# Performance work log

Measured on AMD Instinct MI355X. Metric: run time of the kernel, lower is better.

The kernel has to match this reference:

```python
import jax, jax.numpy as jnp
import numpy as np

FS, R, ULAW = 160, 2, 256  # frame_size, n_samples_per_step, 2**ulaw


def _conv1d(x, w, b):
    # x: [B,C,L], w: [O,I,3], VALID conv (PyTorch Conv1d, no padding)
    y = jax.lax.conv_general_dilated(x, w, (1,), 'VALID',
                                     dimension_numbers=('NCH', 'OIH', 'NCH'))
    return y + b[None, :, None]


def _gru(x, Wih, Whh, bih, bhh):
    # PyTorch GRU (batch_first), gate order r,z,n. x: [B,T,In] -> [B,T,H]
    B = x.shape[0]
    H = Whh.shape[1]
    xW = jnp.einsum('bti,gi->btg', x, Wih) + bih  # precompute input gates [B,T,3H]
    def step(h, xw):
        gh = h @ Whh.T + bhh
        r = jax.nn.sigmoid(xw[:, :H] + gh[:, :H])
        z = jax.nn.sigmoid(xw[:, H:2 * H] + gh[:, H:2 * H])
        n = jnp.tanh(xw[:, 2 * H:] + r * gh[:, 2 * H:])
        h = (1.0 - z) * n + z * h
        return h, h
    h0 = jnp.zeros((B, H), x.dtype)
    _, ys = jax.lax.scan(step, h0, jnp.swapaxes(xW, 0, 1))
    return jnp.swapaxes(ys, 0, 1)


def _mdense(x, w1, w2, b1, b2, f1, f2):
    return jnp.tanh(x @ w1.T + b1) * f1 + jnp.tanh(x @ w2.T + b2) * f2


def setup_inputs() -> dict:
    key = jax.random.key(0)
    ks = jax.random.split(key, 40)
    B, NF, NBF = 64, 15, 20
    T = (NF - 4) * FS  # 1760: two VALID k=3 convs -> 11 frames
    EP, ES, DF, H1, H2 = 64, 128, 128, 384, 16
    IN_A = 3 * ES * R + DF   # 896
    IN_B = H1 + DF           # 512
    p = lambda k, shape, s=0.1: (s * jax.random.normal(k, shape)).astype(jnp.float32)
    d = {
        'in_data': jax.random.randint(ks[0], (B, T, 3), 0, ULAW),
        'features': jax.random.normal(ks[1], (B, NF, NBF), jnp.float32),
        'periods': jax.random.randint(ks[2], (B, NF, 1), 0, 256),
        'targets': jax.random.randint(ks[3], (B, T), 0, ULAW),
        'embed_pitch': p(ks[4], (256, EP)),
        'embed_sig': p(ks[5], (ULAW, ES)),
        'conv1_w': p(ks[6], (DF, EP + NBF, 3)), 'conv1_b': p(ks[7], (DF,)),
        'conv2_w': p(ks[8], (DF, DF, 3)), 'conv2_b': p(ks[9], (DF,)),
        'fd1_w': p(ks[10], (DF, DF)), 'fd1_b': p(ks[11], (DF,)),
        'fd2_w': p(ks[12], (DF, DF)), 'fd2_b': p(ks[13], (DF,)),
        'ga_wih': p(ks[14], (3 * H1, IN_A)), 'ga_whh': p(ks[15], (3 * H1, H1)),
        'ga_bih': p(ks[16], (3 * H1,)), 'ga_bhh': p(ks[17], (3 * H1,)),
        'gb_wih': p(ks[18], (3 * H2, IN_B)), 'gb_whh': p(ks[19], (3 * H2, H2)),
        'gb_bih': p(ks[20], (3 * H2,)), 'gb_bhh': p(ks[21], (3 * H2,)),
        'md1_w1': p(ks[22], (ULAW, H2)), 'md1_w2': p(ks[23], (ULAW, H2)),
        'md1_b1': p(ks[24], (ULAW,)), 'md1_b2': p(ks[25], (ULAW,)),
        'md1_f1': jnp.ones((ULAW,), jnp.float32), 'md1_f2': jnp.ones((ULAW,), jnp.float32),
        'md2_w1': p(ks[26], (ULAW, H2 + ES)), 'md2_w2': p(ks[27], (ULAW, H2 + ES)),
        'md2_b1': p(ks[28], (ULAW,)), 'md2_b2': p(ks[29], (ULAW,)),
        'md2_f1': jnp.ones((ULAW,), jnp.float32), 'md2_f2': jnp.ones((ULAW,), jnp.float32),
    }
    return d


def reference(in_data, features, periods, targets, embed_pitch, embed_sig,
              conv1_w, conv1_b, conv2_w, conv2_b, fd1_w, fd1_b, fd2_w, fd2_b,
              ga_wih, ga_whh, ga_bih, ga_bhh, gb_wih, gb_whh, gb_bih, gb_bhh,
              md1_w1, md1_w2, md1_b1, md1_b2, md1_f1, md1_f2,
              md2_w1, md2_w2, md2_b1, md2_b2, md2_f1, md2_f2):
    B, T = targets.shape
    # frame-rate feature network
    pitch = embed_pitch[periods[..., 0]]                  # [B,15,EP]
    cat = jnp.concatenate([features, pitch], axis=-1)      # [B,15,NBF+EP]
    x = jnp.swapaxes(cat, 1, 2)                            # [B,C,15]
    x = jnp.tanh(_conv1d(x, conv1_w, conv1_b))
    x = jnp.tanh(_conv1d(x, conv2_w, conv2_b))             # [B,DF,11]
    f = jnp.swapaxes(x, 1, 2)
    f = jnp.tanh(f @ fd1_w.T + fd1_b)
    f = jnp.tanh(f @ fd2_w.T + fd2_b)                      # [B,11,DF]
    rep = jnp.repeat(f, FS // R, axis=1)                   # [B,880,DF]
    # sample-rate network (bunched: R samples per step)
    emb = embed_sig[in_data].reshape(B, T, -1).reshape(B, T // R, -1)  # [B,880,3*ES*R]
    rnn_in = jnp.concatenate([emb, rep], axis=-1)
    g1 = _gru(rnn_in, ga_wih, ga_whh, ga_bih, ga_bhh)      # [B,880,H1]
    g2 = _gru(jnp.concatenate([g1, rep], axis=-1), gb_wih, gb_whh, gb_bih, gb_bhh)  # [B,880,H2]
    o1 = _mdense(g2, md1_w1, md1_w2, md1_b1, md1_b2, md1_f1, md1_f2)  # [B,880,ULAW]
    # teacher forcing (p_teacher_forcing = 1.0): even-index targets feed branch 2
    pred_exc = targets[:, 0::R]                            # [B,880]
    ctx = jnp.concatenate([g2, embed_sig[pred_exc]], axis=-1)
    o2 = _mdense(ctx, md2_w1, md2_w2, md2_b1, md2_b2, md2_f1, md2_f2)
    # strided scatter: out[:, ::2]=o1, out[:, 1::2]=o2 == interleave
    out = jnp.stack([o1, o2], axis=2).reshape(B, T, ULAW)
    return out
```

## Files before the change

kernel.cpp:

```cpp
#include <hip/hip_runtime.h>
#include <hip/hip_bf16.h>
#include <hip/hip_fp16.h>

#define NF    15
#define NBF   20
#define TT    1760
#define TS    880
#define EP    64
#define ES    128
#define DF    128
#define H1    384
#define G3    1152
#define INA   896
#define JREP  11

typedef _Float16 h2v __attribute__((ext_vector_type(2)));
typedef unsigned long long u64;

__device__ __forceinline__ float sigmf_(float x){ return 1.0f/(1.0f + __expf(-x)); }
__device__ __forceinline__ float tanhf_(float x){ return 2.0f/(1.0f + __expf(-2.0f*x)) - 1.0f; }
__device__ __forceinline__ h2v bc_h2(unsigned u){ return __builtin_bit_cast(h2v, u); }
__device__ __forceinline__ float fdot2_(h2v a, h2v b, float c){
#if __has_builtin(__builtin_amdgcn_fdot2)
  return __builtin_amdgcn_fdot2(a, b, c, false);
#else
  return c + (float)a[0]*(float)b[0] + (float)a[1]*(float)b[1];
#endif
}
__device__ __forceinline__ unsigned pk2_(float a, float b){
#if __has_builtin(__builtin_amdgcn_cvt_pkrtz)
  return __builtin_bit_cast(unsigned, __builtin_amdgcn_cvt_pkrtz(a, b));
#else
  unsigned lo = (unsigned)__builtin_bit_cast(unsigned short, (_Float16)a);
  unsigned hi = (unsigned)__builtin_bit_cast(unsigned short, (_Float16)b);
  return lo | (hi << 16);
#endif
}
__device__ __forceinline__ void bar_lgkm(){
  asm volatile("s_waitcnt lgkmcnt(0)" ::: "memory");
  __builtin_amdgcn_s_barrier();
  __builtin_amdgcn_sched_barrier(0);
}

__global__ __launch_bounds__(128) void k_frame(const float* feat, const int* periods, const float* embp,
   const float* c1w, const float* c1b, const float* c2w, const float* c2b,
   const float* f1w, const float* f1b, const float* f2w, const float* f2b, float* fout)
{
  __shared__ float cat[NF*84];
  __shared__ float x1[13*DF];
  __shared__ float x2[JREP*DF];
  int b = blockIdx.x, tid = threadIdx.x;
  for (int idx = tid; idx < NF*84; idx += 128){
    int j = idx/84, c = idx%84;
    cat[idx] = (c < NBF) ? feat[(b*NF+j)*NBF + c]
                         : embp[periods[b*NF+j]*EP + (c-NBF)];
  }
  __syncthreads();
  int o = tid;
  for (int p = 0; p < 13; ++p){
    float acc = c1b[o];
    for (int kk = 0; kk < 3; ++kk)
      for (int c = 0; c < 84; ++c)
        acc += cat[(p+kk)*84 + c] * c1w[(o*84+c)*3+kk];
    x1[p*DF+o] = tanhf_(acc);
  }
  __syncthreads();
  for (int p = 0; p < JREP; ++p){
    float acc = c2b[o];
    for (int kk = 0; kk < 3; ++kk)
      for (int c = 0; c < DF; ++c)
        acc += x1[(p+kk)*DF+c] * c2w[(o*DF+c)*3+kk];
    x2[p*DF+o] = tanhf_(acc);
  }
  __syncthreads();
  for (int p = 0; p < JREP; ++p){
    float acc = f1b[o];
    for (int c = 0; c < DF; ++c) acc += x2[p*DF+c]*f1w[o*DF+c];
    x1[p*DF+o] = tanhf_(acc);
  }
  __syncthreads();
  for (int p = 0; p < JREP; ++p){
    float acc = f2b[o];
    for (int c = 0; c < DF; ++c) acc += x1[p*DF+c]*f2w[o*DF+c];
    fout[(b*JREP+p)*DF+o] = tanhf_(acc);
  }
}

__global__ __launch_bounds__(256) void k_wpack5(const float* whh, _Float16* wpk){
  int o = blockIdx.x*256 + threadIdx.x;
  int hu = o & 1;
  int c  = (o >> 1) & 3;
  int idx = o >> 3;
  int tid = idx % 768;
  int n   = (idx / 768) % 18;
  int hf  = idx / (768*18);
  int i = tid % 384, u = tid / 384;
  int gd = n*4 + c;
  int m = gd / 12, dc = gd % 12;
  int pos  = (dc % 2) + 2*(dc / 6);
  int gate = (dc % 6) >> 1;
  int j = hf*96 + u*48 + (4*m + pos)*2 + hu;
  wpk[o] = (_Float16)whh[(gate*H1 + i)*H1 + j];
}

__global__ __launch_bounds__(256) void k_tables(const float* wih, const float* emb, float* GA){
  __shared__ float Wl[64*129];
  int k = blockIdx.x/18, g0 = (blockIdx.x%18)*64;
  int tid = threadIdx.x;
  for (int idx = tid; idx < 64*128; idx += 256){
    int gg = idx>>7, c = idx&127;
    Wl[gg*129+c] = wih[(size_t)(g0+gg)*INA + k*128 + c];
  }
  __syncthreads();
  int vv = tid>>6, gg = tid&63;
  for (int v = vv; v < 256; v += 4){
    const float* e = emb + (size_t)v*ES;
    float acc = 0.f;
    for (int c = 0; c < 128; ++c) acc += e[c]*Wl[gg*129+c];
    GA[(size_t)(k*256+v)*G3 + g0+gg] = acc;
  }
}

__global__ __launch_bounds__(256) void k_xwrepA(const float* wih, const float* f,
                                                const float* bih, const float* bhh, float* xwA){
  __shared__ float Wl[64*129];
  int g0 = blockIdx.x*64, tid = threadIdx.x;
  for (int idx = tid; idx < 64*128; idx += 256){
    int gg = idx>>7, c = idx&127;
    Wl[gg*129+c] = wih[(size_t)(g0+gg)*INA + 768 + c];
  }
  __syncthreads();
  int vv = tid>>6, gg = tid&63; int g = g0+gg;
  float badd = bih[g] + (g < 768 ? bhh[g] : 0.f);
  for (int row = vv; row < 64*JREP; row += 4){
    const float* fr = f + (size_t)row*DF;
    float acc = badd;
    for (int c = 0; c < 128; ++c) acc += fr[c]*Wl[gg*129+c];
    xwA[(size_t)row*G3 + g] = acc;
  }
}

__global__ __launch_bounds__(256) void k_xwrepB(const float* wih, const float* f,
                                                const float* bih, const float* bhh, float* xwB){
  __shared__ float Wl[48*129];
  int b = blockIdx.x, tid = threadIdx.x;
  for (int idx = tid; idx < 48*128; idx += 256){
    int r = idx>>7, c = idx&127;
    Wl[r*129+c] = wih[r*512 + 384 + c];
  }
  __syncthreads();
  for (int idx = tid; idx < JREP*48; idx += 256){
    int j = idx/48, r = idx%48;
    const float* fr = f + (size_t)(b*JREP+j)*DF;
    float acc = bih[r] + (r < 32 ? bhh[r] : 0.f);
    for (int c = 0; c < 128; ++c) acc += fr[c]*Wl[r*129+c];
    xwB[(size_t)(b*JREP+j)*48 + r] = acc;
  }
}

__global__ __launch_bounds__(256) void k_t2(const float* w1, const float* w2, const float* emb, float* T2){
  __shared__ float Wl[64*129];
  int tbl = blockIdx.x>>2; int c0 = (blockIdx.x&3)*64; int tid = threadIdx.x;
  const float* w = tbl ? w2 : w1;
  for (int idx = tid; idx < 64*128; idx += 256){
    int cc = idx>>7, e = idx&127;
    Wl[cc*129+e] = w[(c0+cc)*144 + 16 + e];
  }
  __syncthreads();
  int vv = tid>>6, cc = tid&63;
  for (int v = vv; v < 256; v += 4){
    const float* e = emb + (size_t)v*ES;
    float acc = 0.f;
    for (int c = 0; c < 128; ++c) acc += e[c]*Wl[cc*129+c];
    T2[tbl*65536 + v*256 + c0+cc] = acc;
  }
}

#define LD18(n) uint4 d##n = wsrc[(size_t)(n)*768];
#define Q2(A,B,C, q2) { \
  h2v hA = hh[jb2 + (q2)*2],     hB = hh[jb2 + (q2)*2 + 1]; \
  ar = fdot2_(hA, bc_h2(A.x), ar); ar = fdot2_(hB, bc_h2(A.y), ar); \
  az = fdot2_(hA, bc_h2(A.z), az); az = fdot2_(hB, bc_h2(A.w), az); \
  an = fdot2_(hA, bc_h2(B.x), an); an = fdot2_(hB, bc_h2(B.y), an); \
  h2v hC = hh[jb2 + (q2)*2 + 2], hD = hh[jb2 + (q2)*2 + 3]; \
  ar = fdot2_(hC, bc_h2(B.z), ar); ar = fdot2_(hD, bc_h2(B.w), ar); \
  az = fdot2_(hC, bc_h2(C.x), az); az = fdot2_(hD, bc_h2(C.y), az); \
  an = fdot2_(hC, bc_h2(C.z), an); an = fdot2_(hD, bc_h2(C.w), an); }
#define DOTS12 \
  Q2(d0,d1,d2,0) Q2(d3,d4,d5,2) Q2(d6,d7,d8,4) \
  Q2(d9,d10,d11,6) Q2(d12,d13,d14,8) Q2(d15,d16,d17,10)

#define PL2(na, nb_, p) { u64 w2 = __hip_atomic_load((const u64*)(p), __ATOMIC_RELAXED, __HIP_MEMORY_SCOPE_AGENT); \
  rv##na = (unsigned)w2; rv##nb_ = (unsigned)(w2 >> 32); \
  ok &= ((rv##na & 1023u) == tg) & ((rv##nb_ & 1023u) == tg); }

__global__ __launch_bounds__(768, 3) void k_scanA13(const int* __restrict__ in_data,
        const float* __restrict__ GA, const float* __restrict__ xwA,
        const uint4* __restrict__ wpk, const float* __restrict__ bhh,
        unsigned* __restrict__ g1u, unsigned* pbuf)
{
  __shared__ __align__(16) unsigned h16u[48];
  __shared__ __align__(8)  float pg[3][2][384];
  __shared__ __align__(8)  float xwb[2][G3];
  __shared__ int indr[2][8];
  const int P = blockIdx.x;
  const int b = P & 63, hf = P >> 6;
  const int tid = threadIdx.x;
  const int i  = tid % 384;
  const int u  = tid / 384;
  const int jb2 = u * 24;
  const int* ind_b = in_data + (size_t)b*TT*3;

  const uint4* wsrc = wpk + (size_t)(hf*18)*768 + tid;
  LD18(0) LD18(1) LD18(2) LD18(3) LD18(4) LD18(5) LD18(6) LD18(7) LD18(8)
  LD18(9) LD18(10) LD18(11) LD18(12) LD18(13) LD18(14) LD18(15) LD18(16) LD18(17)

  const bool isGat = (tid < 576);
  const int  c0 = 2*tid, c1 = 2*tid + 1;
  const bool isPub = (tid >= 96 && tid < 672);
  const int  po0 = 2*(tid - 96);

  float hreg0 = 0.f, hreg1 = 0.f, bn0 = 0.f, bn1 = 0.f;
  if (tid < 48){
    bn0 = bhh[768 + hf*96 + 2*tid];
    bn1 = bhh[768 + hf*96 + 2*tid + 1];
    h16u[tid] = 0u;
  }
  if (isGat){
    float s0 = xwA[(size_t)(b*JREP)*G3 + c0];
    float s1 = xwA[(size_t)(b*JREP)*G3 + c1];
    #pragma unroll
    for (int k2 = 0; k2 < 6; ++k2){
      int v = ind_b[k2];
      s0 += GA[((size_t)k2*256 + v)*G3 + c0];
      s1 += GA[((size_t)k2*256 + v)*G3 + c1];
    }
    xwb[0][c0] = s0; xwb[0][c1] = s1;
  }
  if (tid >= 576 && tid < 582) indr[1][tid-576] = ind_b[6 + (tid-576)];

  unsigned* pbo = pbuf + ((size_t)(b*4 + hf)*2)*G3;
  const int pf1 = (hf+1)&3, pf2 = (hf+2)&3, pf3 = (hf+3)&3;
  const unsigned* pb1 = pbuf + ((size_t)(b*4 + pf1)*2)*G3 + hf*96 + 2*(tid<48?tid:0);
  const unsigned* pb2 = pbuf + ((size_t)(b*4 + pf2)*2)*G3 + hf*96 + 2*(tid<48?tid:0);
  const unsigned* pb3 = pbuf + ((size_t)(b*4 + pf3)*2)*G3 + hf*96 + 2*(tid<48?tid:0);
  const h2v* hh = (const h2v*)h16u;
  __syncthreads();

  for (int t = 0; t < TS; ++t){
    const int nb = t & 1;
    const int tp = t + 1;
    float ga0=0.f,ga1=0.f,ga2=0.f,ga3=0.f,ga4=0.f,ga5=0.f,gx0=0.f;
    float gb0=0.f,gb1=0.f,gb2=0.f,gb3=0.f,gb4=0.f,gb5=0.f,gx1=0.f;
    if (tp < TS && isGat){
      int v0=indr[tp&1][0], v1=indr[tp&1][1], v2=indr[tp&1][2];
      int v3=indr[tp&1][3], v4=indr[tp&1][4], v5=indr[tp&1][5];
      const float* xwr = xwA + ((size_t)(b*JREP) + tp/80)*G3;
      ga0 = GA[((size_t)0*256 + v0)*G3 + c0]; gb0 = GA[((size_t)0*256 + v0)*G3 + c1];
      ga1 = GA[((size_t)1*256 + v1)*G3 + c0]; gb1 = GA[((size_t)1*256 + v1)*G3 + c1];
      ga2 = GA[((size_t)2*256 + v2)*G3 + c0]; gb2 = GA[((size_t)2*256 + v2)*G3 + c1];
      ga3 = GA[((size_t)3*256 + v3)*G3 + c0]; gb3 = GA[((size_t)3*256 + v3)*G3 + c1];
      ga4 = GA[((size_t)4*256 + v4)*G3 + c0]; gb4 = GA[((size_t)4*256 + v4)*G3 + c1];
      ga5 = GA[((size_t)5*256 + v5)*G3 + c0]; gb5 = GA[((size_t)5*256 + v5)*G3 + c1];
      gx0 = xwr[c0]; gx1 = xwr[c1];
    }
    int iv = 0;
    const int stg = t + 2;
    const bool doStg = (tid >= 576 && tid < 582 && stg < TS);
    if (doStg) iv = ind_b[6*stg + (tid-576)];
    float ar=0.f, az=0.f, an=0.f;
    DOTS12
    pg[0][u][i] = ar; pg[1][u][i] = az; pg[2][u][i] = an;
    if (tp < TS && isGat){
      xwb[tp&1][c0] = ga0+ga1+ga2+ga3+ga4+ga5+gx0;
      xwb[tp&1][c1] = gb0+gb1+gb2+gb3+gb4+gb5+gx1;
    }
    if (doStg) indr[t&1][tid-576] = iv;
    bar_lgkm();
    if (isPub){
      int g = po0/384, ii = po0 - g*384;
      float2 p0 = *(const float2*)&pg[g][0][ii];
      float2 p1 = *(const float2*)&pg[g][1][ii];
      float v0 = p0.x + p1.x, v1 = p0.y + p1.y;
      unsigned tw0 = (__builtin_bit_cast(unsigned, v0) & 0xFFFFFC00u) | (unsigned)(t & 1023);
      unsigned tw1 = (__builtin_bit_cast(unsigned, v1) & 0xFFFFFC00u) | (unsigned)(t & 1023);
      unsigned* dst = pbo + (size_t)nb*G3 + po0;
      __hip_atomic_store(dst,     tw0, __ATOMIC_RELAXED, __HIP_MEMORY_SCOPE_AGENT);
      __hip_atomic_store(dst + 1, tw1, __ATOMIC_RELAXED, __HIP_MEMORY_SCOPE_AGENT);
    } else if (tid < 48){
      const unsigned tg = (unsigned)t & 1023u;
      const unsigned* q1 = pb1 + (size_t)nb*G3;
      const unsigned* q2 = pb2 + (size_t)nb*G3;
      const unsigned* q3 = pb3 + (size_t)nb*G3;
      unsigned rv0,rv1,rv2,rv3,rv4,rv5,rv6,rv7,rv8;
      unsigned rv9,rv10,rv11,rv12,rv13,rv14,rv15,rv16,rv17;
      bool ok;
      do {
        ok = true;
        PL2(0,1,   q1+0) PL2(2,3,   q1+384) PL2(4,5,   q1+768)
        PL2(6,7,   q2+0) PL2(8,9,   q2+384) PL2(10,11, q2+768)
        PL2(12,13, q3+0) PL2(14,15, q3+384) PL2(16,17, q3+768)
        if (!ok) __builtin_amdgcn_s_sleep(1);
      } while (!ok);
      __builtin_amdgcn_sched_barrier(0);
      #define FV(n) __builtin_bit_cast(float, rv##n & 0xFFFFFC00u)
      int i0 = hf*96 + 2*tid;
      float2 o0 = *(const float2*)&pg[0][0][i0];  float2 o0b = *(const float2*)&pg[0][1][i0];
      float2 o1 = *(const float2*)&pg[1][0][i0];  float2 o1b = *(const float2*)&pg[1][1][i0];
      float2 o2 = *(const float2*)&pg[2][0][i0];  float2 o2b = *(const float2*)&pg[2][1][i0];
      float2 xr = *(const float2*)&xwb[nb][i0];
      float2 xz = *(const float2*)&xwb[nb][384 + i0];
      float2 xn = *(const float2*)&xwb[nb][768 + i0];
      float R0 = o0.x + o0b.x + FV(0)  + FV(6)  + FV(12) + xr.x;
      float R1 = o0.y + o0b.y + FV(1)  + FV(7)  + FV(13) + xr.y;
      float Z0 = o1.x + o1b.x + FV(2)  + FV(8)  + FV(14) + xz.x;
      float Z1 = o1.y + o1b.y + FV(3)  + FV(9)  + FV(15) + xz.y;
      float G0 = o2.x + o2b.x + FV(4)  + FV(10) + FV(16) + bn0;
      float G1 = o2.y + o2b.y + FV(5)  + FV(11) + FV(17) + bn1;
      #undef FV
      float rr0 = sigmf_(R0), zz0 = sigmf_(Z0);
      float nn0 = tanhf_(xn.x + rr0*G0);
      float h0 = (1.f - zz0)*nn0 + zz0*hreg0; hreg0 = h0;
      float rr1 = sigmf_(R1), zz1 = sigmf_(Z1);
      float nn1 = tanhf_(xn.y + rr1*G1);
      float h1 = (1.f - zz1)*nn1 + zz1*hreg1; hreg1 = h1;
      unsigned pack = pk2_(h0, h1);
      h16u[tid] = pack;
      g1u[((size_t)b*TS + t)*192 + hf*48 + tid] = pack;
    }
    bar_lgkm();
  }
}

__global__ __launch_bounds__(256) void k_xwB(const unsigned* g1u, const float* wih,
                                             const float* xwrB, float* xwB){
  __shared__ __align__(16) unsigned gl[16*194];
  __shared__ __align__(16) unsigned wl[48*194];
  int bi = blockIdx.x; int b = bi/55; int t0 = (bi%55)*16; int tid = threadIdx.x;
  for (int idx = tid; idx < 48*192; idx += 256){
    int r = idx/192, cp = idx%192;
    wl[r*194+cp] = pk2_(wih[r*512 + 2*cp], wih[r*512 + 2*cp + 1]);
  }
  for (int idx = tid; idx < 16*192; idx += 256){
    int tt = idx/192, c = idx%192;
    gl[tt*194+c] = g1u[((size_t)b*TS + t0+tt)*192 + c];
  }
  __syncthreads();
  int rr = tid>>4, tt = tid&15;
  int t = t0+tt;
  const float* xr = xwrB + ((size_t)(b*JREP) + t/80)*48;
  const h2v* gp = (const h2v*)&gl[tt*194];
  for (int rb = 0; rb < 3; ++rb){
    int r = rb*16 + rr;
    const h2v* wp_ = (const h2v*)&wl[r*194];
    float acc = 0.f;
    #pragma unroll 8
    for (int c = 0; c < 192; ++c) acc = fdot2_(gp[c], wp_[c], acc);
    xwB[((size_t)b*TS + t)*48 + r] = acc + xr[r];
  }
}

__global__ __launch_bounds__(64) void k_scanB(const float* xwB, const float* whh,
                                              const float* bhh, float* g2){
  int b = blockIdx.x, tid = threadIdx.x;
  float w0=0,w1=0,w2=0,w3=0,w4=0,w5=0,w6=0,w7=0;
  float w8=0,w9=0,w10=0,w11=0,w12=0,w13=0,w14=0,w15=0;
  if (tid < 48){
    const float* wr = whh + tid*16;
    w0=wr[0];w1=wr[1];w2=wr[2];w3=wr[3];w4=wr[4];w5=wr[5];w6=wr[6];w7=wr[7];
    w8=wr[8];w9=wr[9];w10=wr[10];w11=wr[11];w12=wr[12];w13=wr[13];w14=wr[14];w15=wr[15];
  }
  float bng = (tid < 16) ? bhh[32 + tid] : 0.f;
  float hv = 0.f;
  float xw_n = (tid < 48) ? xwB[(size_t)b*TS*48 + tid] : 0.f;
  for (int t = 0; t < TS; ++t){
    float xw = xw_n;
    if (t+1 < TS && tid < 48) xw_n = xwB[((size_t)b*TS + t+1)*48 + tid];
    float gh = 0.f;
    gh += w0 *__shfl(hv, 0, 64);  gh += w1 *__shfl(hv, 1, 64);
    gh += w2 *__shfl(hv, 2, 64);  gh += w3 *__shfl(hv, 3, 64);
    gh += w4 *__shfl(hv, 4, 64);  gh += w5 *__shfl(hv, 5, 64);
    gh += w6 *__shfl(hv, 6, 64);  gh += w7 *__shfl(hv, 7, 64);
    gh += w8 *__shfl(hv, 8, 64);  gh += w9 *__shfl(hv, 9, 64);
    gh += w10*__shfl(hv,10, 64);  gh += w11*__shfl(hv,11, 64);
    gh += w12*__shfl(hv,12, 64);  gh += w13*__shfl(hv,13, 64);
    gh += w14*__shfl(hv,14, 64);  gh += w15*__shfl(hv,15, 64);
    float val = xw + gh;
    float zv  = __shfl(val, (tid+16) & 63, 64);
    float xn_ = __shfl(xw,  (tid+32) & 63, 64);
    float gn_ = __shfl(gh,  (tid+32) & 63, 64) + bng;
    if (tid < 16){
      float r = sigmf_(val), z = sigmf_(zv);
      float n = tanhf_(xn_ + r*gn_);
      hv = (1.f - z)*n + z*hv;
      g2[((size_t)b*TS + t)*16 + tid] = hv;
    }
  }
}

__global__ __launch_bounds__(256) void k_out(const float* g2, const int* targets, const float* T2,
    const float* m1w1, const float* m1w2, const float* m1b1, const float* m1b2,
    const float* m1f1, const float* m1f2,
    const float* m2w1, const float* m2w2, const float* m2b1, const float* m2b2,
    const float* m2f1, const float* m2f2, float* out)
{
  __shared__ float wA[256*17], wB[256*17], wC[256*17], wD[256*17];
  __shared__ float g2l[16*16];
  int bi = blockIdx.x; int b = bi/55; int t0 = (bi%55)*16; int c = threadIdx.x;
  for (int d = 0; d < 16; ++d){
    wA[c*17+d] = m1w1[c*16+d];  wB[c*17+d] = m1w2[c*16+d];
    wC[c*17+d] = m2w1[c*144+d]; wD[c*17+d] = m2w2[c*144+d];
  }
  { int tt = c>>4, d = c&15; g2l[c] = g2[((size_t)b*TS + t0+tt)*16 + d]; }
  __syncthreads();
  float b1a = m1b1[c], b2a = m1b2[c], f1a = m1f1[c], f2a = m1f2[c];
  float b1b = m2b1[c], b2b = m2b2[c], f1b = m2f1[c], f2b = m2f2[c];
  for (int tt = 0; tt < 16; ++tt){
    int t = t0+tt;
    float d1 = b1a, d2 = b2a, e1 = b1b, e2 = b2b;
    for (int d = 0; d < 16; ++d){
      float g = g2l[tt*16+d];
      d1 += g*wA[c*17+d]; d2 += g*wB[c*17+d];
      e1 += g*wC[c*17+d]; e2 += g*wD[c*17+d];
    }
    int v = targets[b*TT + 2*t];
    e1 += T2[v*256+c]; e2 += T2[65536 + v*256+c];
    float o1 = f1a*tanhf_(d1) + f2a*tanhf_(d2);
    float o2 = f1b*tanhf_(e1) + f2b*tanhf_(e2);
    size_t base = ((size_t)b*TS + t)*2*256;
    out[base + c]       = o1;
    out[base + 256 + c] = o2;
  }
}

extern "C" void kernel_launch(void* const* d_in, const int* in_sizes, int n_in,
                              void* d_out, int out_size, void* d_ws, size_t ws_size,
                              hipStream_t stream) {
  const int*   in_data = (const int*)  d_in[0];
  const float* feat    = (const float*)d_in[1];
  const int*   periods = (const int*)  d_in[2];
  const int*   targets = (const int*)  d_in[3];
  const float* embp    = (const float*)d_in[4];
  const float* embs    = (const float*)d_in[5];
  const float* c1w = (const float*)d_in[6];  const float* c1b = (const float*)d_in[7];
  const float* c2w = (const float*)d_in[8];  const float* c2b = (const float*)d_in[9];
  const float* f1w = (const float*)d_in[10]; const float* f1b = (const float*)d_in[11];
  const float* f2w = (const float*)d_in[12]; const float* f2b = (const float*)d_in[13];
  const float* ga_wih = (const float*)d_in[14]; const float* ga_whh = (const float*)d_in[15];
  const float* ga_bih = (const float*)d_in[16]; const float* ga_bhh = (const float*)d_in[17];
  const float* gb_wih = (const float*)d_in[18]; const float* gb_whh = (const float*)d_in[19];
  const float* gb_bih = (const float*)d_in[20]; const float* gb_bhh = (const float*)d_in[21];
  const float* m1w1 = (const float*)d_in[22]; const float* m1w2 = (const float*)d_in[23];
  const float* m1b1 = (const float*)d_in[24]; const float* m1b2 = (const float*)d_in[25];
  const float* m1f1 = (const float*)d_in[26]; const float* m1f2 = (const float*)d_in[27];
  const float* m2w1 = (const float*)d_in[28]; const float* m2w2 = (const float*)d_in[29];
  const float* m2b1 = (const float*)d_in[30]; const float* m2b2 = (const float*)d_in[31];
  const float* m2f1 = (const float*)d_in[32]; const float* m2f2 = (const float*)d_in[33];
  float* out = (float*)d_out;

  float* GA     = (float*)d_ws;
  float* xWrepA = GA     + 1769472;
  float* xWrepB = xWrepA + 811008;
  float* fbuf   = xWrepB + 33792;
  float* xWB    = fbuf   + 90112;
  float* g2buf  = xWB    + 2703360;
  float* T2     = g2buf  + 901120;
  _Float16* Wpk = (_Float16*)(T2 + 131072);
  unsigned* pbuf = (unsigned*)(Wpk + 442368);
  _Float16* g1  = (_Float16*)d_out;

  (void)hipMemsetAsync(pbuf, 0xFF, 589824*sizeof(unsigned), stream);
  hipLaunchKernelGGL(k_frame, dim3(64), dim3(128), 0, stream,
                     feat, periods, embp, c1w, c1b, c2w, c2b, f1w, f1b, f2w, f2b, fbuf);
  hipLaunchKernelGGL(k_wpack5, dim3(1728), dim3(256), 0, stream, ga_whh, Wpk);
  hipLaunchKernelGGL(k_tables, dim3(108), dim3(256), 0, stream, ga_wih, embs, GA);
  hipLaunchKernelGGL(k_t2, dim3(8), dim3(256), 0, stream, m2w1, m2w2, embs, T2);
  hipLaunchKernelGGL(k_xwrepA, dim3(18), dim3(256), 0, stream, ga_wih, fbuf, ga_bih, ga_bhh, xWrepA);
  hipLaunchKernelGGL(k_xwrepB, dim3(64), dim3(256), 0, stream, gb_wih, fbuf, gb_bih, gb_bhh, xWrepB);
  hipLaunchKernelGGL(k_scanA13, dim3(256), dim3(768), 0, stream,
                     in_data, GA, xWrepA, (const uint4*)Wpk, ga_bhh,
                     (unsigned*)g1, pbuf);
  hipLaunchKernelGGL(k_xwB, dim3(64*55), dim3(256), 0, stream,
                     (const unsigned*)g1, gb_wih, xWrepB, xWB);
  hipLaunchKernelGGL(k_scanB, dim3(64), dim3(64), 0, stream, xWB, gb_whh, gb_bhh, g2buf);
  hipLaunchKernelGGL(k_out, dim3(64*55), dim3(256), 0, stream,
                     g2buf, targets, T2, m1w1, m1w2, m1b1, m1b2, m1f1, m1f2,
                     m2w1, m2w2, m2b1, m2b2, m2f1, m2f2, out);
}
```

Before: 3.645 ms.

## Fuse GRU-B input projection into scan A and merge setup kernels

Each GRU-A block now computes partial projections of its slice of the hidden state onto the GRU-B input weights inside the recurrent loop, one step late, using idle threads 48-95. It writes per-quarter partial sums that scan B adds up. This removes the g1 round trip through memory and the separate k_xwB kernel. The six small setup kernels are also merged into two launches with block-index dispatch. The trade-offs are extra shared memory and work on the latency-critical scan-A loop, and four partial-sum reads per step in scan B.

```diff
diff --git a/kernel.cpp b/kernel.cpp
--- a/kernel.cpp
+++ b/kernel.cpp
@@ -42,137 +42,148 @@
   __builtin_amdgcn_sched_barrier(0);
 }
 
-__global__ __launch_bounds__(128) void k_frame(const float* feat, const int* periods, const float* embp,
+__global__ __launch_bounds__(256) void k_setupA(const float* feat, const int* periods, const float* embp,
    const float* c1w, const float* c1b, const float* c2w, const float* c2b,
-   const float* f1w, const float* f1b, const float* f2w, const float* f2b, float* fout)
+   const float* f1w, const float* f1b, const float* f2w, const float* f2b, float* fout,
+   const float* whh, _Float16* wpk,
+   const float* wih, const float* emb, float* GA,
+   const float* m2w1, const float* m2w2, float* T2)
 {
-  __shared__ float cat[NF*84];
-  __shared__ float x1[13*DF];
-  __shared__ float x2[JREP*DF];
-  int b = blockIdx.x, tid = threadIdx.x;
-  for (int idx = tid; idx < NF*84; idx += 128){
-    int j = idx/84, c = idx%84;
-    cat[idx] = (c < NBF) ? feat[(b*NF+j)*NBF + c]
-                         : embp[periods[b*NF+j]*EP + (c-NBF)];
-  }
-  __syncthreads();
-  int o = tid;
-  for (int p = 0; p < 13; ++p){
-    float acc = c1b[o];
-    for (int kk = 0; kk < 3; ++kk)
-      for (int c = 0; c < 84; ++c)
-        acc += cat[(p+kk)*84 + c] * c1w[(o*84+c)*3+kk];
-    x1[p*DF+o] = tanhf_(acc);
-  }
-  __syncthreads();
-  for (int p = 0; p < JREP; ++p){
-    float acc = c2b[o];
-    for (int kk = 0; kk < 3; ++kk)
-      for (int c = 0; c < DF; ++c)
-        acc += x1[(p+kk)*DF+c] * c2w[(o*DF+c)*3+kk];
-    x2[p*DF+o] = tanhf_(acc);
-  }
-  __syncthreads();
-  for (int p = 0; p < JREP; ++p){
-    float acc = f1b[o];
-    for (int c = 0; c < DF; ++c) acc += x2[p*DF+c]*f1w[o*DF+c];
-    x1[p*DF+o] = tanhf_(acc);
-  }
-  __syncthreads();
-  for (int p = 0; p < JREP; ++p){
-    float acc = f2b[o];
-    for (int c = 0; c < DF; ++c) acc += x1[p*DF+c]*f2w[o*DF+c];
-    fout[(b*JREP+p)*DF+o] = tanhf_(acc);
-  }
-}
-
-__global__ __launch_bounds__(256) void k_wpack5(const float* whh, _Float16* wpk){
-  int o = blockIdx.x*256 + threadIdx.x;
-  int hu = o & 1;
-  int c  = (o >> 1) & 3;
-  int idx = o >> 3;
-  int tid = idx % 768;
-  int n   = (idx / 768) % 18;
-  int hf  = idx / (768*18);
-  int i = tid % 384, u = tid / 384;
-  int gd = n*4 + c;
-  int m = gd / 12, dc = gd % 12;
-  int pos  = (dc % 2) + 2*(dc / 6);
-  int gate = (dc % 6) >> 1;
-  int j = hf*96 + u*48 + (4*m + pos)*2 + hu;
-  wpk[o] = (_Float16)whh[(gate*H1 + i)*H1 + j];
-}
-
-__global__ __launch_bounds__(256) void k_tables(const float* wih, const float* emb, float* GA){
+  __shared__ float sh[8256];
+  const int bi = blockIdx.x, tid = threadIdx.x;
+  if (bi < 64){
+    float* cat = sh;
+    float* x1  = sh + 1260;
+    float* x2  = sh + 2924;
+    int b = bi;
+    for (int idx = tid; idx < NF*84; idx += 256){
+      int j = idx/84, c = idx%84;
+      cat[idx] = (c < NBF) ? feat[(b*NF+j)*NBF + c]
+                           : embp[periods[b*NF+j]*EP + (c-NBF)];
+    }
+    __syncthreads();
+    int o = tid;
+    if (o < DF){
+      for (int p = 0; p < 13; ++p){
+        float acc = c1b[o];
+        for (int kk = 0; kk < 3; ++kk)
+          for (int c = 0; c < 84; ++c)
+            acc += cat[(p+kk)*84 + c] * c1w[(o*84+c)*3+kk];
+        x1[p*DF+o] = tanhf_(acc);
+      }
+    }
+    __syncthreads();
+    if (o < DF){
+      for (int p = 0; p < JREP; ++p){
+        float acc = c2b[o];
+        for (int kk = 0; kk < 3; ++kk)
+          for (int c = 0; c < DF; ++c)
+            acc += x1[(p+kk)*DF+c] * c2w[(o*DF+c)*3+kk];
+        x2[p*DF+o] = tanhf_(acc);
+      }
+    }
+    __syncthreads();
+    if (o < DF){
+      for (int p = 0; p < JREP; ++p){
+        float acc = f1b[o];
+        for (int c = 0; c < DF; ++c) acc += x2[p*DF+c]*f1w[o*DF+c];
+        x1[p*DF+o] = tanhf_(acc);
+      }
+    }
+    __syncthreads();
+    if (o < DF){
+      for (int p = 0; p < JREP; ++p){
+        float acc = f2b[o];
+        for (int c = 0; c < DF; ++c) acc += x1[p*DF+c]*f2w[o*DF+c];
+        fout[(b*JREP+p)*DF+o] = tanhf_(acc);
+      }
+    }
+  } else if (bi < 1792){
+    int o = (bi-64)*256 + tid;
+    int hu = o & 1;
+    int c  = (o >> 1) & 3;
+    int idx = o >> 3;
+    int t768 = idx % 768;
+    int n    = (idx / 768) % 18;
+    int hf   = idx / (768*18);
+    int i = t768 % 384, u = t768 / 384;
+    int gd = n*4 + c;
+    int m = gd / 12, dc = gd % 12;
+    int pos  = (dc % 2) + 2*(dc / 6);
+    int gate = (dc % 6) >> 1;
+    int j = hf*96 + u*48 + (4*m + pos)*2 + hu;
+    wpk[o] = (_Float16)whh[(gate*H1 + i)*H1 + j];
+  } else if (bi < 1900){
+    float* Wl = sh;
+    int bb = bi - 1792;
+    int k = bb/18, g0 = (bb%18)*64;
+    for (int idx = tid; idx < 64*128; idx += 256){
+      int gg = idx>>7, c = idx&127;
+      Wl[gg*129+c] = wih[(size_t)(g0+gg)*INA + k*128 + c];
+    }
+    __syncthreads();
+    int vv = tid>>6, gg = tid&63;
+    for (int v = vv; v < 256; v += 4){
+      const float* e = emb + (size_t)v*ES;
+      float acc = 0.f;
+      for (int c = 0; c < 128; ++c) acc += e[c]*Wl[gg*129+c];
+      GA[(size_t)(k*256+v)*G3 + g0+gg] = acc;
+    }
+  } else {
+    float* Wl = sh;
+    int bb = bi - 1900;
+    int tbl = bb>>2; int c0 = (bb&3)*64;
+    const float* w = tbl ? m2w2 : m2w1;
+    for (int idx = tid; idx < 64*128; idx += 256){
+      int cc = idx>>7, e = idx&127;
+      Wl[cc*129+e] = w[(c0+cc)*144 + 16 + e];
+    }
+    __syncthreads();
+    int vv = tid>>6, cc = tid&63;
+    for (int v = vv; v < 256; v += 4){
+      const float* e = emb + (size_t)v*ES;
+      float acc = 0.f;
+      for (int c = 0; c < 128; ++c) acc += e[c]*Wl[cc*129+c];
+      T2[tbl*65536 + v*256 + c0+cc] = acc;
+    }
+  }
+}
+
+__global__ __launch_bounds__(256) void k_setupB(const float* wihA, const float* f,
+        const float* bihA, const float* bhhA, float* xwA,
+        const float* wihB, const float* bihB, const float* bhhB, float* xwB)
+{
   __shared__ float Wl[64*129];
-  int k = blockIdx.x/18, g0 = (blockIdx.x%18)*64;
-  int tid = threadIdx.x;
-  for (int idx = tid; idx < 64*128; idx += 256){
-    int gg = idx>>7, c = idx&127;
-    Wl[gg*129+c] = wih[(size_t)(g0+gg)*INA + k*128 + c];
-  }
-  __syncthreads();
-  int vv = tid>>6, gg = tid&63;
-  for (int v = vv; v < 256; v += 4){
-    const float* e = emb + (size_t)v*ES;
-    float acc = 0.f;
-    for (int c = 0; c < 128; ++c) acc += e[c]*Wl[gg*129+c];
-    GA[(size_t)(k*256+v)*G3 + g0+gg] = acc;
-  }
-}
-
-__global__ __launch_bounds__(256) void k_xwrepA(const float* wih, const float* f,
-                                                const float* bih, const float* bhh, float* xwA){
-  __shared__ float Wl[64*129];
-  int g0 = blockIdx.x*64, tid = threadIdx.x;
-  for (int idx = tid; idx < 64*128; idx += 256){
-    int gg = idx>>7, c = idx&127;
-    Wl[gg*129+c] = wih[(size_t)(g0+gg)*INA + 768 + c];
-  }
-  __syncthreads();
-  int vv = tid>>6, gg = tid&63; int g = g0+gg;
-  float badd = bih[g] + (g < 768 ? bhh[g] : 0.f);
-  for (int row = vv; row < 64*JREP; row += 4){
-    const float* fr = f + (size_t)row*DF;
-    float acc = badd;
-    for (int c = 0; c < 128; ++c) acc += fr[c]*Wl[gg*129+c];
-    xwA[(size_t)row*G3 + g] = acc;
-  }
-}
-
-__global__ __launch_bounds__(256) void k_xwrepB(const float* wih, const float* f,
-                                                const float* bih, const float* bhh, float* xwB){
-  __shared__ float Wl[48*129];
-  int b = blockIdx.x, tid = threadIdx.x;
-  for (int idx = tid; idx < 48*128; idx += 256){
-    int r = idx>>7, c = idx&127;
-    Wl[r*129+c] = wih[r*512 + 384 + c];
-  }
-  __syncthreads();
-  for (int idx = tid; idx < JREP*48; idx += 256){
-    int j = idx/48, r = idx%48;
-    const float* fr = f + (size_t)(b*JREP+j)*DF;
-    float acc = bih[r] + (r < 32 ? bhh[r] : 0.f);
-    for (int c = 0; c < 128; ++c) acc += fr[c]*Wl[r*129+c];
-    xwB[(size_t)(b*JREP+j)*48 + r] = acc;
-  }
-}
-
-__global__ __launch_bounds__(256) void k_t2(const float* w1, const float* w2, const float* emb, float* T2){
-  __shared__ float Wl[64*129];
-  int tbl = blockIdx.x>>2; int c0 = (blockIdx.x&3)*64; int tid = threadIdx.x;
-  const float* w = tbl ? w2 : w1;
-  for (int idx = tid; idx < 64*128; idx += 256){
-    int cc = idx>>7, e = idx&127;
-    Wl[cc*129+e] = w[(c0+cc)*144 + 16 + e];
-  }
-  __syncthreads();
-  int vv = tid>>6, cc = tid&63;
-  for (int v = vv; v < 256; v += 4){
-    const float* e = emb + (size_t)v*ES;
-    float acc = 0.f;
-    for (int c = 0; c < 128; ++c) acc += e[c]*Wl[cc*129+c];
-    T2[tbl*65536 + v*256 + c0+cc] = acc;
+  const int bi = blockIdx.x, tid = threadIdx.x;
+  if (bi < 18){
+    int g0 = bi*64;
+    for (int idx = tid; idx < 64*128; idx += 256){
+      int gg = idx>>7, c = idx&127;
+      Wl[gg*129+c] = wihA[(size_t)(g0+gg)*INA + 768 + c];
+    }
+    __syncthreads();
+    int vv = tid>>6, gg = tid&63; int g = g0+gg;
+    float badd = bihA[g] + (g < 768 ? bhhA[g] : 0.f);
+    for (int row = vv; row < 64*JREP; row += 4){
+      const float* fr = f + (size_t)row*DF;
+      float acc = badd;
+      for (int c = 0; c < 128; ++c) acc += fr[c]*Wl[gg*129+c];
+      xwA[(size_t)row*G3 + g] = acc;
+    }
+  } else {
+    int b = bi - 18;
+    for (int idx = tid; idx < 48*128; idx += 256){
+      int r = idx>>7, c = idx&127;
+      Wl[r*129+c] = wihB[r*512 + 384 + c];
+    }
+    __syncthreads();
+    for (int idx = tid; idx < JREP*48; idx += 256){
+      int j = idx/48, r = idx%48;
+      const float* fr = f + (size_t)(b*JREP+j)*DF;
+      float acc = bihB[r] + (r < 32 ? bhhB[r] : 0.f);
+      for (int c = 0; c < 128; ++c) acc += fr[c]*Wl[r*129+c];
+      xwB[(size_t)(b*JREP+j)*48 + r] = acc;
+    }
   }
 }
 
@@ -194,14 +205,15 @@
   rv##na = (unsigned)w2; rv##nb_ = (unsigned)(w2 >> 32); \
   ok &= ((rv##na & 1023u) == tg) & ((rv##nb_ & 1023u) == tg); }
 
-__global__ __launch_bounds__(768, 3) void k_scanA13(const int* __restrict__ in_data,
+__global__ __launch_bounds__(768, 3) void k_scanA14(const int* __restrict__ in_data,
         const float* __restrict__ GA, const float* __restrict__ xwA,
         const uint4* __restrict__ wpk, const float* __restrict__ bhh,
-        unsigned* __restrict__ g1u, unsigned* pbuf)
+        const float* __restrict__ wihB, unsigned* pbuf, float* __restrict__ pxb)
 {
   __shared__ __align__(16) unsigned h16u[48];
   __shared__ __align__(8)  float pg[3][2][384];
   __shared__ __align__(8)  float xwb[2][G3];
+  __shared__ __align__(8)  unsigned wlB[48*49];
   __shared__ int indr[2][8];
   const int P = blockIdx.x;
   const int b = P & 63, hf = P >> 6;
@@ -215,10 +227,17 @@
   LD18(0) LD18(1) LD18(2) LD18(3) LD18(4) LD18(5) LD18(6) LD18(7) LD18(8)
   LD18(9) LD18(10) LD18(11) LD18(12) LD18(13) LD18(14) LD18(15) LD18(16) LD18(17)
 
+  for (int idx = tid; idx < 48*48; idx += 768){
+    int r = idx/48, k = idx%48;
+    wlB[r*49+k] = pk2_(wihB[r*512 + hf*96 + 2*k], wihB[r*512 + hf*96 + 2*k + 1]);
+  }
+
   const bool isGat = (tid < 576);
   const int  c0 = 2*tid, c1 = 2*tid + 1;
   const bool isPub = (tid >= 96 && tid < 672);
   const int  po0 = 2*(tid - 96);
+  const bool isPxb = (tid >= 48 && tid < 96);
+  float* pxbBase = pxb + (size_t)(b*4 + hf)*TS*48 + (tid - 48);
 
   float hreg0 = 0.f, hreg1 = 0.f, bn0 = 0.f, bn1 = 0.f;
   if (tid < 48){
@@ -271,6 +290,13 @@
     float ar=0.f, az=0.f, an=0.f;
     DOTS12
     pg[0][u][i] = ar; pg[1][u][i] = az; pg[2][u][i] = an;
+    if (isPxb && t > 0){
+      int r = tid - 48;
+      float acc = 0.f;
+      #pragma unroll 8
+      for (int k = 0; k < 48; ++k) acc = fdot2_(hh[k], bc_h2(wlB[r*49+k]), acc);
+      pxbBase[(size_t)(t-1)*48] = acc;
+    }
     if (tp < TS && isGat){
       xwb[tp&1][c0] = ga0+ga1+ga2+ga3+ga4+ga5+gx0;
       xwb[tp&1][c1] = gb0+gb1+gb2+gb3+gb4+gb5+gx1;
@@ -324,44 +350,21 @@
       float rr1 = sigmf_(R1), zz1 = sigmf_(Z1);
       float nn1 = tanhf_(xn.y + rr1*G1);
       float h1 = (1.f - zz1)*nn1 + zz1*hreg1; hreg1 = h1;
-      unsigned pack = pk2_(h0, h1);
-      h16u[tid] = pack;
-      g1u[((size_t)b*TS + t)*192 + hf*48 + tid] = pack;
+      h16u[tid] = pk2_(h0, h1);
     }
     bar_lgkm();
   }
-}
-
-__global__ __launch_bounds__(256) void k_xwB(const unsigned* g1u, const float* wih,
-                                             const float* xwrB, float* xwB){
-  __shared__ __align__(16) unsigned gl[16*194];
-  __shared__ __align__(16) unsigned wl[48*194];
-  int bi = blockIdx.x; int b = bi/55; int t0 = (bi%55)*16; int tid = threadIdx.x;
-  for (int idx = tid; idx < 48*192; idx += 256){
-    int r = idx/192, cp = idx%192;
-    wl[r*194+cp] = pk2_(wih[r*512 + 2*cp], wih[r*512 + 2*cp + 1]);
-  }
-  for (int idx = tid; idx < 16*192; idx += 256){
-    int tt = idx/192, c = idx%192;
-    gl[tt*194+c] = g1u[((size_t)b*TS + t0+tt)*192 + c];
-  }
-  __syncthreads();
-  int rr = tid>>4, tt = tid&15;
-  int t = t0+tt;
-  const float* xr = xwrB + ((size_t)(b*JREP) + t/80)*48;
-  const h2v* gp = (const h2v*)&gl[tt*194];
-  for (int rb = 0; rb < 3; ++rb){
-    int r = rb*16 + rr;
-    const h2v* wp_ = (const h2v*)&wl[r*194];
+  if (isPxb){
+    int r = tid - 48;
     float acc = 0.f;
     #pragma unroll 8
-    for (int c = 0; c < 192; ++c) acc = fdot2_(gp[c], wp_[c], acc);
-    xwB[((size_t)b*TS + t)*48 + r] = acc + xr[r];
-  }
-}
-
-__global__ __launch_bounds__(64) void k_scanB(const float* xwB, const float* whh,
-                                              const float* bhh, float* g2){
+    for (int k = 0; k < 48; ++k) acc = fdot2_(hh[k], bc_h2(wlB[r*49+k]), acc);
+    pxbBase[(size_t)(TS-1)*48] = acc;
+  }
+}
+
+__global__ __launch_bounds__(64) void k_scanB(const float* pxb, const float* xwrB,
+                                              const float* whh, const float* bhh, float* g2){
   int b = blockIdx.x, tid = threadIdx.x;
   float w0=0,w1=0,w2=0,w3=0,w4=0,w5=0,w6=0,w7=0;
   float w8=0,w9=0,w10=0,w11=0,w12=0,w13=0,w14=0,w15=0;
@@ -371,11 +374,19 @@
     w8=wr[8];w9=wr[9];w10=wr[10];w11=wr[11];w12=wr[12];w13=wr[13];w14=wr[14];w15=wr[15];
   }
   float bng = (tid < 16) ? bhh[32 + tid] : 0.f;
+  const float* p0 = pxb + (size_t)(b*4+0)*TS*48 + tid;
+  const float* p1 = pxb + (size_t)(b*4+1)*TS*48 + tid;
+  const float* p2 = pxb + (size_t)(b*4+2)*TS*48 + tid;
+  const float* p3 = pxb + (size_t)(b*4+3)*TS*48 + tid;
+  const float* xr = xwrB + (size_t)(b*JREP)*48 + tid;
   float hv = 0.f;
-  float xw_n = (tid < 48) ? xwB[(size_t)b*TS*48 + tid] : 0.f;
+  float xw_n = 0.f;
+  if (tid < 48) xw_n = p0[0] + p1[0] + p2[0] + p3[0] + xr[0];
   for (int t = 0; t < TS; ++t){
     float xw = xw_n;
-    if (t+1 < TS && tid < 48) xw_n = xwB[((size_t)b*TS + t+1)*48 + tid];
+    if (t+1 < TS && tid < 48)
+      xw_n = p0[(size_t)(t+1)*48] + p1[(size_t)(t+1)*48] + p2[(size_t)(t+1)*48]
+           + p3[(size_t)(t+1)*48] + xr[(size_t)((t+1)/80)*48];
     float gh = 0.f;
     gh += w0 *__shfl(hv, 0, 64);  gh += w1 *__shfl(hv, 1, 64);
     gh += w2 *__shfl(hv, 2, 64);  gh += w3 *__shfl(hv, 3, 64);
@@ -462,27 +473,24 @@
   float* xWrepA = GA     + 1769472;
   float* xWrepB = xWrepA + 811008;
   float* fbuf   = xWrepB + 33792;
-  float* xWB    = fbuf   + 90112;
-  float* g2buf  = xWB    + 2703360;
+  float* g2buf  = fbuf   + 90112;
   float* T2     = g2buf  + 901120;
   _Float16* Wpk = (_Float16*)(T2 + 131072);
   unsigned* pbuf = (unsigned*)(Wpk + 442368);
-  _Float16* g1  = (_Float16*)d_out;
+  float* pxb    = (float*)d_out;
 
   (void)hipMemsetAsync(pbuf, 0xFF, 589824*sizeof(unsigned), stream);
-  hipLaunchKernelGGL(k_frame, dim3(64), dim3(128), 0, stream,
-                     feat, periods, embp, c1w, c1b, c2w, c2b, f1w, f1b, f2w, f2b, fbuf);
-  hipLaunchKernelGGL(k_wpack5, dim3(1728), dim3(256), 0, stream, ga_whh, Wpk);
-  hipLaunchKernelGGL(k_tables, dim3(108), dim3(256), 0, stream, ga_wih, embs, GA);
-  hipLaunchKernelGGL(k_t2, dim3(8), dim3(256), 0, stream, m2w1, m2w2, embs, T2);
-  hipLaunchKernelGGL(k_xwrepA, dim3(18), dim3(256), 0, stream, ga_wih, fbuf, ga_bih, ga_bhh, xWrepA);
-  hipLaunchKernelGGL(k_xwrepB, dim3(64), dim3(256), 0, stream, gb_wih, fbuf, gb_bih, gb_bhh, xWrepB);
-  hipLaunchKernelGGL(k_scanA13, dim3(256), dim3(768), 0, stream,
+  hipLaunchKernelGGL(k_setupA, dim3(1908), dim3(256), 0, stream,
+                     feat, periods, embp, c1w, c1b, c2w, c2b, f1w, f1b, f2w, f2b, fbuf,
+                     ga_whh, Wpk, ga_wih, embs, GA, m2w1, m2w2, T2);
+  hipLaunchKernelGGL(k_setupB, dim3(82), dim3(256), 0, stream,
+                     ga_wih, fbuf, ga_bih, ga_bhh, xWrepA,
+                     gb_wih, gb_bih, gb_bhh, xWrepB);
+  hipLaunchKernelGGL(k_scanA14, dim3(256), dim3(768), 0, stream,
                      in_data, GA, xWrepA, (const uint4*)Wpk, ga_bhh,
-                     (unsigned*)g1, pbuf);
-  hipLaunchKernelGGL(k_xwB, dim3(64*55), dim3(256), 0, stream,
-                     (const unsigned*)g1, gb_wih, xWrepB, xWB);
-  hipLaunchKernelGGL(k_scanB, dim3(64), dim3(64), 0, stream, xWB, gb_whh, gb_bhh, g2buf);
+                     gb_wih, pbuf, pxb);
+  hipLaunchKernelGGL(k_scanB, dim3(64), dim3(64), 0, stream,
+                     pxb, xWrepB, gb_whh, gb_bhh, g2buf);
   hipLaunchKernelGGL(k_out, dim3(64*55), dim3(256), 0, stream,
                      g2buf, targets, T2, m1w1, m1w2, m1b1, m1b2, m1f1, m1f2,
                      m2w1, m2w2, m2b1, m2b2, m2f1, m2f2, out);
```

Result: no change. 3.629 ms (-0.4%).
